# Kernel tuning notes

Hardware: AMD Instinct MI355X
Metric: run time of the kernel (lower is better)

## Reference

```python
import jax, jax.numpy as jnp
import numpy as np

C, T, V, H, DQ = 64, 128, 25, 3, 32  # channels, frames, joints, heads, qkv_dim
EPS = 1e-5
LRELU_SLOPE = 0.1


def pos_embed(channels, num_frames, num_joints):
    # DSTA-Net style sinusoidal Pos_Embed: position index is the joint id, tiled over frames
    pos = np.tile(np.arange(num_joints, dtype=np.float32), num_frames)[:, None]  # (T*V, 1)
    div = np.exp(np.arange(0, channels, 2, dtype=np.float32) * -(np.log(10000.0) / channels))
    pe = np.zeros((num_frames * num_joints, channels), dtype=np.float32)
    pe[:, 0::2] = np.sin(pos * div)
    pe[:, 1::2] = np.cos(pos * div)
    pe = pe.reshape(num_frames, num_joints, channels).transpose(2, 0, 1)[None]  # (1, C, T, V)
    return jnp.asarray(pe)


def batchnorm2d(x, gamma, beta):
    # training-mode BN over (N, T, V) per channel, biased variance (torch default)
    m = x.mean(axis=(0, 2, 3), keepdims=True)
    v = x.var(axis=(0, 2, 3), keepdims=True)
    return (x - m) * jax.lax.rsqrt(v + EPS) * gamma[None, :, None, None] + beta[None, :, None, None]


def setup_inputs() -> dict:
    key = jax.random.key(0)
    ks = jax.random.split(key, 4)
    N = 64
    return {
        "x": jax.random.normal(ks[0], (N, C, T, V), jnp.float32),
        "Wqkv": jax.random.normal(ks[1], (2 * H * DQ, C), jnp.float32) * 0.05,   # 1x1 conv weight
        "bqkv": jnp.zeros((2 * H * DQ,), jnp.float32),
        "alphas": jnp.ones((1, H, 1, 1), jnp.float32),
        "att0s": jax.random.uniform(ks[2], (1, H, V, V), jnp.float32) / V,
        "Wout": jax.random.normal(ks[3], (C, H * C, 1, 5), jnp.float32) * 0.02,  # (1,5) temporal conv
        "bout": jnp.zeros((C,), jnp.float32),
        "gamma": jnp.ones((C,), jnp.float32),
        "beta": jnp.zeros((C,), jnp.float32),
    }


def reference(x, Wqkv, bqkv, alphas, att0s, Wout, bout, gamma, beta):
    N = x.shape[0]
    xs = x + pos_embed(C, T, V)                                   # pes(x) + x
    qk = jnp.einsum('nctv,oc->notv', xs, Wqkv) + bqkv[None, :, None, None]
    qk = qk.reshape(N, 2 * H, DQ, T, V)
    q, k = qk[:, :H], qk[:, H:]
    # tanh-gated joint-attention, no softmax
    att = jnp.tanh(jnp.einsum('nhctu,nhctv->nhuv', q, k) / (DQ * T)) * alphas + att0s
    y = jnp.einsum('nctu,nhuv->nhctv', x, att).reshape(N, H * C, T, V)
    y = jax.lax.conv_general_dilated(
        y, Wout, window_strides=(1, 1), padding=((0, 0), (2, 2)),
        dimension_numbers=('NCHW', 'OIHW', 'NCHW')) + bout[None, :, None, None]
    y = batchnorm2d(y, gamma, beta)
    return jax.nn.leaky_relu(y + x, LRELU_SLOPE)                  # ress is identity (in==out)
```

## Files before the change

### kernel.cpp

```cpp
#include <hip/hip_runtime.h>
#include <hip/hip_bf16.h>


#define WS_ATT    0
#define WS_STATS  120000
#define WS_WBF    120128
#define WS_WP     150848
#define WS_BP     156992
#define WS_PE     157184
#define WS_SPART  158784
#define WS_ATTBF  166976

typedef __attribute__((ext_vector_type(8))) short short8;
typedef __attribute__((ext_vector_type(4))) float floatx4;

__device__ __forceinline__ float us2f(unsigned short u) {
    union { unsigned int i; float f; } w; w.i = ((unsigned int)u) << 16; return w.f;
}
__device__ __forceinline__ unsigned short f2us(float f) {
    __hip_bfloat16_raw r = __float2bfloat16(f); return r.x;
}

__device__ __forceinline__ int swz(int col, int byteoff) {
    return col * 128 + ((((byteoff >> 4) ^ (col & 7)) << 4) | (byteoff & 15));
}

__device__ __forceinline__ void bar_lgkm() {
    asm volatile("s_waitcnt lgkmcnt(0)" ::: "memory");
    __builtin_amdgcn_s_barrier();
}

__global__ void k_wprep(const float* __restrict__ Wout, const float* __restrict__ Wqkv,
                        const float* __restrict__ bqkv, unsigned short* __restrict__ Abf,
                        unsigned short* __restrict__ Wp, float* __restrict__ bp,
                        float* __restrict__ pe)
{
    int i = blockIdx.x * 256 + threadIdx.x;
    if (i < 61440) {
        int tap = i / 12288, rem = i % 12288;
        int o = rem / 192, hc = rem % 192;
        Abf[i] = f2us(Wout[o * 960 + hc * 5 + tap]);
    } else if (i < 73728) {
        int j = i - 61440;
        int np = j >> 6, c = j & 63;
        int h = np >> 6, qk = (np >> 5) & 1, cp = np & 31;
        Wp[j] = f2us(Wqkv[(qk * 96 + h * 32 + cp) * 64 + c]);
    } else if (i < 73920) {
        int np = i - 73728;
        int h = np >> 6, qk = (np >> 5) & 1, cp = np & 31;
        bp[np] = bqkv[qk * 96 + h * 32 + cp];
    } else if (i < 75520) {
        int e = i - 73920;
        int c = e / 25, v = e % 25;
        int ii = c >> 1;
        float d = expf(-(float)(2 * ii) * (9.210340371976184f / 64.0f));
        float a = (float)v * d;
        pe[e] = (c & 1) ? cosf(a) : sinf(a);
    }
}

#define CPAD 112

__global__ __launch_bounds__(256, 2) void k_att(
    const float* __restrict__ x, const unsigned short* __restrict__ Wp,
    const float* __restrict__ bp, const float* __restrict__ peg,
    float* __restrict__ att_raw)
{
    __shared__ unsigned short xs_s[2][CPAD * 64];
    __shared__ unsigned short qk_s[3 * CPAD * 64];
    __shared__ float pe_s[1600];

    const int tid  = threadIdx.x;
    const int lane = tid & 63, wv = tid >> 6;
    const int l16  = lane & 15, quad = lane >> 4;
    const int n    = blockIdx.y;
    const int tb0  = blockIdx.x * 16;

    const int col_a = lane;
    const int col_b = 64 + lane;
    const int va = (col_a < 25) ? col_a : (col_a < 50 ? col_a - 25 : col_a - 50);
    const int vb = (col_b < 75) ? col_b - 50 : col_b - 75;
    char* qkb = (char*)qk_s;

    float ra0[8], ra1[8], rb0[8], rb1[8];

#define LOADCH(CH) do {                                                         \
    const int g0_ = (tb0 + (CH) * 4) * 25;                                      \
    _Pragma("unroll")                                                           \
    for (int cp8 = 0; cp8 < 8; ++cp8) {                                         \
        const float* xp0_ = x + (size_t)(n * 64 + (wv * 8 + cp8) * 2) * 3200 + g0_; \
        const float* xp1_ = xp0_ + 3200;                                        \
        ra0[cp8] = xp0_[col_a]; ra1[cp8] = xp1_[col_a];                         \
        if (lane < 36) { rb0[cp8] = xp0_[col_b]; rb1[cp8] = xp1_[col_b]; }      \
    } } while (0)

    LOADCH(0);

    for (int e = tid; e < 1600; e += 256) pe_s[e] = peg[e];

    short8 afrag[3][2];
    float  biasr[3][4];
    #pragma unroll
    for (int mt = 0; mt < 3; ++mt) {
        int row = (3 * wv + mt) * 16 + l16;
        #pragma unroll
        for (int kk = 0; kk < 2; ++kk)
            afrag[mt][kk] = *(const short8*)(Wp + row * 64 + kk * 32 + quad * 8);
        #pragma unroll
        for (int reg = 0; reg < 4; ++reg)
            biasr[mt][reg] = bp[(3 * wv + mt) * 16 + quad * 4 + reg];
    }

    floatx4 qacc[3][2][2];
    #pragma unroll
    for (int h = 0; h < 3; ++h)
        #pragma unroll
        for (int a = 0; a < 2; ++a)
            #pragma unroll
            for (int b = 0; b < 2; ++b)
                qacc[h][a][b] = (floatx4){0.0f, 0.0f, 0.0f, 0.0f};

    bar_lgkm();

    #pragma unroll
    for (int ch = 0; ch < 4; ++ch) {
        char* xsb = (char*)xs_s[ch & 1];

        #pragma unroll
        for (int cp8 = 0; cp8 < 8; ++cp8) {
            const int cpair = wv * 8 + cp8, c0 = cpair * 2;
            unsigned int pk =
                (unsigned int)f2us(ra0[cp8] + pe_s[c0 * 25 + va]) |
                ((unsigned int)f2us(ra1[cp8] + pe_s[c0 * 25 + 25 + va]) << 16);
            *(unsigned int*)(xsb + swz(col_a, cpair * 4)) = pk;
            if (lane < 36) {
                pk = (unsigned int)f2us(rb0[cp8] + pe_s[c0 * 25 + vb]) |
                     ((unsigned int)f2us(rb1[cp8] + pe_s[c0 * 25 + 25 + vb]) << 16);
                *(unsigned int*)(xsb + swz(col_b, cpair * 4)) = pk;
            }
        }
        if (ch < 3) LOADCH(ch + 1);
        bar_lgkm();

        #pragma unroll
        for (int nt = 0; nt < 7; ++nt) {
            const int col = nt * 16 + l16;
            short8 b0 = *(const short8*)(xsb + swz(col, quad * 16));
            short8 b1 = *(const short8*)(xsb + swz(col, 64 + quad * 16));
            #pragma unroll
            for (int mt = 0; mt < 3; ++mt) {
                floatx4 acc = (floatx4){0.0f, 0.0f, 0.0f, 0.0f};
                acc = __builtin_amdgcn_mfma_f32_16x16x32_bf16(afrag[mt][0], b0, acc, 0, 0, 0);
                acc = __builtin_amdgcn_mfma_f32_16x16x32_bf16(afrag[mt][1], b1, acc, 0, 0, 0);
                const int np  = (3 * wv + mt) * 16 + quad * 4;
                const int h   = np >> 6;
                const int off = (np & 63) * 2;
                unsigned long long pk =
                      (unsigned long long)f2us(acc[0] + biasr[mt][0])
                    | ((unsigned long long)f2us(acc[1] + biasr[mt][1]) << 16)
                    | ((unsigned long long)f2us(acc[2] + biasr[mt][2]) << 32)
                    | ((unsigned long long)f2us(acc[3] + biasr[mt][3]) << 48);
                *(unsigned long long*)(qkb + h * (CPAD * 128) + swz(col, off)) = pk;
            }
        }
        bar_lgkm();

        const int tcol = wv * 25;
        #pragma unroll
        for (int h = 0; h < 3; ++h) {
            char* qh = qkb + h * (CPAD * 128);
            short8 qa0 = *(const short8*)(qh + swz(tcol + l16,      quad * 16));
            short8 qa1 = *(const short8*)(qh + swz(tcol + 16 + l16, quad * 16));
            short8 kb0 = *(const short8*)(qh + swz(tcol + l16,      64 + quad * 16));
            short8 kb1 = *(const short8*)(qh + swz(tcol + 16 + l16, 64 + quad * 16));
            qacc[h][0][0] = __builtin_amdgcn_mfma_f32_16x16x32_bf16(qa0, kb0, qacc[h][0][0], 0, 0, 0);
            qacc[h][0][1] = __builtin_amdgcn_mfma_f32_16x16x32_bf16(qa0, kb1, qacc[h][0][1], 0, 0, 0);
            qacc[h][1][0] = __builtin_amdgcn_mfma_f32_16x16x32_bf16(qa1, kb0, qacc[h][1][0], 0, 0, 0);
            qacc[h][1][1] = __builtin_amdgcn_mfma_f32_16x16x32_bf16(qa1, kb1, qacc[h][1][1], 0, 0, 0);
        }
    }

    __syncthreads();
    float* att_s = (float*)qk_s;
    for (int e = tid; e < 1875; e += 256) att_s[e] = 0.0f;
    __syncthreads();
    #pragma unroll
    for (int h = 0; h < 3; ++h) {
        #pragma unroll
        for (int ut = 0; ut < 2; ++ut) {
            #pragma unroll
            for (int vt = 0; vt < 2; ++vt) {
                const int v = vt * 16 + l16;
                if (v < 25) {
                    const int ub = ut * 16 + quad * 4;
                    #pragma unroll
                    for (int reg = 0; reg < 4; ++reg) {
                        const int u = ub + reg;
                        if (u < 25)
                            atomicAdd(&att_s[h * 625 + u * 25 + v], qacc[h][ut][vt][reg]);
                    }
                }
            }
        }
    }
    __syncthreads();
    for (int e = tid; e < 1875; e += 256)
        atomicAdd(&att_raw[(size_t)n * 1875 + e], att_s[e]);
}

__global__ void k_attfin(const float* __restrict__ att_raw,
                         unsigned short* __restrict__ attbf,
                         const float* __restrict__ alphas,
                         const float* __restrict__ att0s)
{
    int idx = blockIdx.x * 256 + threadIdx.x;
    if (idx >= 64 * 3 * 25 * 40) return;
    int u = idx % 40;
    int r = idx / 40;
    int v = r % 25;
    int nh = r / 25;
    int h = nh % 3;
    unsigned short val = 0;
    if (u < 25) {
        float a = att_raw[nh * 625 + u * 25 + v];
        val = f2us(tanhf(a * (1.0f / 4096.0f)) * alphas[h] + att0s[h * 625 + u * 25 + v]);
    }
    attbf[idx] = val;
}

__global__ __launch_bounds__(256, 3) void k_conv(
    const float* __restrict__ x, const unsigned short* __restrict__ Abf,
    const float* __restrict__ bout, const unsigned short* __restrict__ attbf,
    float* __restrict__ out, float* __restrict__ spart)
{
    __shared__ unsigned short yT[11136];
    __shared__ unsigned short x_sb[4096];
    __shared__ unsigned short attT[3000];
    __shared__ float stats_s[128];

    const int tid = threadIdx.x;
    const int n = blockIdx.y;
    const int t0 = blockIdx.x * 2;
    char* xsb = (char*)x_sb;

    if (tid < 128) stats_s[tid] = 0.0f;

    for (int e = tid; e < 896; e += 256) {
        int c = e / 14, r = e % 14;
        int t = r / 7, u = 25 + r % 7;
        *(unsigned short*)(xsb + swz(c, (t * 32 + u) * 2)) = 0;
    }
    for (int e = tid; e < 1600; e += 256) {
        int c = e / 25, j = e % 25;
        const float2 xv = *(const float2*)(x + (size_t)(n * 64 + c) * 3200 + t0 * 25 + 2 * j);
        int i0 = 2 * j, i1 = i0 + 1;
        int p0 = (i0 / 25) * 32 + (i0 % 25);
        int p1 = (i1 / 25) * 32 + (i1 % 25);
        *(unsigned short*)(xsb + swz(c, p0 * 2)) = f2us(xv.x);
        *(unsigned short*)(xsb + swz(c, p1 * 2)) = f2us(xv.y);
    }
    {
        const uint4* src = (const uint4*)(attbf + (size_t)n * 3000);
        uint4* dst = (uint4*)attT;
        for (int e = tid; e < 375; e += 256) dst[e] = src[e];
    }
    for (int e = tid; e < 1536; e += 256) {
        int t = e / 768, r = e % 768;
        int vi = r / 192, hc = r % 192;
        int vv = (vi < 2) ? vi : (25 + vi);
        int phys = (t * 29 + vv) * 192 + (((hc >> 3) ^ (vv & 7)) << 3) + (hc & 7);
        yT[phys] = 0;
    }
    __syncthreads();

    const int lane = tid & 63, wv = tid >> 6;
    const int quad = lane >> 4, l16 = lane & 15;

    {
        const int c0 = wv * 16;
        const int crow = c0 + l16;
        short8 af[2];
        #pragma unroll
        for (int t = 0; t < 2; ++t)
            af[t] = *(const short8*)(xsb + swz(crow, (t * 32 + quad * 8) * 2));
        short8 bfr[3][2];
        #pragma unroll
        for (int h = 0; h < 3; ++h)
            #pragma unroll
            for (int nt = 0; nt < 2; ++nt) {
                int v = nt * 16 + l16; if (v > 24) v = 24;
                bfr[h][nt] = *(const short8*)&attT[(h * 25 + v) * 40 + quad * 8];
            }
        #pragma unroll
        for (int t = 0; t < 2; ++t)
            #pragma unroll
            for (int h = 0; h < 3; ++h)
                #pragma unroll
                for (int nt = 0; nt < 2; ++nt) {
                    floatx4 d = (floatx4){0.0f, 0.0f, 0.0f, 0.0f};
                    d = __builtin_amdgcn_mfma_f32_16x16x32_bf16(af[t], bfr[h][nt], d, 0, 0, 0);
                    const int v = nt * 16 + l16;
                    if (v < 25) {
                        const int vv = v + 2;
                        const int hc = h * 64 + c0 + quad * 4;
                        const int phys = (t * 29 + vv) * 192 + (((hc >> 3) ^ (vv & 7)) << 3) + (hc & 7);
                        unsigned long long pk =
                              (unsigned long long)f2us(d[0])
                            | ((unsigned long long)f2us(d[1]) << 16)
                            | ((unsigned long long)f2us(d[2]) << 32)
                            | ((unsigned long long)f2us(d[3]) << 48);
                        *(unsigned long long*)&yT[phys] = pk;
                    }
                }
    }

    const int o0 = wv * 16;
    short8 areg[5][6];
    const unsigned short* apb = Abf + (o0 + l16) * 192 + quad * 8;
    #pragma unroll
    for (int tap = 0; tap < 5; ++tap)
        #pragma unroll
        for (int kk = 0; kk < 6; ++kk)
            areg[tap][kk] = *(const short8*)(apb + tap * 12288 + kk * 32);
    float bo[4];
    #pragma unroll
    for (int reg = 0; reg < 4; ++reg) bo[reg] = bout[o0 + quad * 4 + reg];

    bar_lgkm();

    float s1[4] = {0, 0, 0, 0}, s2[4] = {0, 0, 0, 0};
    #pragma unroll
    for (int nt = 0; nt < 4; ++nt) {
        int col = nt * 16 + l16;
        const bool ok = col < 50;
        if (col > 49) col = 49;
        const int tc = col / 25, vc = col % 25;
        floatx4 acc = (floatx4){0.0f, 0.0f, 0.0f, 0.0f};
        #pragma unroll
        for (int tap = 0; tap < 5; ++tap) {
            const int vv = vc + tap;
            const int ro = (tc * 29 + vv) * 192, vx = vv & 7;
            #pragma unroll
            for (int kk = 0; kk < 6; ++kk) {
                short8 b = *(const short8*)&yT[ro + (((kk * 4 + quad) ^ vx) << 3)];
                acc = __builtin_amdgcn_mfma_f32_16x16x32_bf16(areg[tap][kk], b, acc, 0, 0, 0);
            }
        }
        float vr[4];
        #pragma unroll
        for (int reg = 0; reg < 4; ++reg)
            vr[reg] = ok ? acc[reg] + bo[reg] : 0.0f;
        if (ok) {
            float* op = out + (size_t)(n * 64 + o0 + quad * 4) * 3200 + (t0 + tc) * 25 + vc;
            #pragma unroll
            for (int reg = 0; reg < 4; ++reg)
                op[(size_t)reg * 3200] = vr[reg];
        }
        #pragma unroll
        for (int reg = 0; reg < 4; ++reg) {
            s1[reg] += vr[reg];
            s2[reg] = fmaf(vr[reg], vr[reg], s2[reg]);
        }
    }

    #pragma unroll
    for (int reg = 0; reg < 4; ++reg) {
        float a = s1[reg], b = s2[reg];
        #pragma unroll
        for (int m = 1; m < 16; m <<= 1) {
            a += __shfl_xor(a, m);
            b += __shfl_xor(b, m);
        }
        if (l16 == 0) {
            atomicAdd(&stats_s[o0 + quad * 4 + reg], a);
            atomicAdd(&stats_s[64 + o0 + quad * 4 + reg], b);
        }
    }
    __syncthreads();
    if (tid < 128)
        atomicAdd(&spart[(size_t)blockIdx.x * 128 + tid], stats_s[tid]);
}

__global__ void k_statsred(const float* __restrict__ spart, float* __restrict__ stats)
{
    int o = threadIdx.x;
    float s = 0.0f;
    #pragma unroll 8
    for (int t = 0; t < 64; ++t) s += spart[t * 128 + o];
    stats[o] = s;
}

__global__ void k_final(const float* __restrict__ stats, const float4* __restrict__ x4,
                        const float* __restrict__ gamma, const float* __restrict__ beta,
                        float4* __restrict__ out4)
{
    int idx = blockIdx.x * 256 + threadIdx.x;
    if (idx >= 3276800) return;
    int o = (idx / 800) & 63;
    const float inv = 1.0f / 204800.0f;
    float m   = stats[o] * inv;
    float ex2 = stats[64 + o] * inv;
    float var = ex2 - m * m;
    float r = rsqrtf(var + 1e-5f);
    float g = gamma[o], bb = beta[o];
    float4 v = out4[idx];
    float4 xx = x4[idx];
    float4 res;
    float t;
    t = (v.x - m) * r * g + bb + xx.x; res.x = fmaxf(t, 0.1f * t);
    t = (v.y - m) * r * g + bb + xx.y; res.y = fmaxf(t, 0.1f * t);
    t = (v.z - m) * r * g + bb + xx.z; res.z = fmaxf(t, 0.1f * t);
    t = (v.w - m) * r * g + bb + xx.w; res.w = fmaxf(t, 0.1f * t);
    out4[idx] = res;
}

extern "C" void kernel_launch(void* const* d_in, const int* in_sizes, int n_in,
                              void* d_out, int out_size, void* d_ws, size_t ws_size,
                              hipStream_t stream)
{
    const float* x      = (const float*)d_in[0];
    const float* Wqkv   = (const float*)d_in[1];
    const float* bqkv   = (const float*)d_in[2];
    const float* alphas = (const float*)d_in[3];
    const float* att0s  = (const float*)d_in[4];
    const float* Wout   = (const float*)d_in[5];
    const float* bout   = (const float*)d_in[6];
    const float* gamma  = (const float*)d_in[7];
    const float* beta   = (const float*)d_in[8];
    float* ws  = (float*)d_ws;
    float* out = (float*)d_out;
    unsigned short* Abf   = (unsigned short*)(ws + WS_WBF);
    unsigned short* Wp    = (unsigned short*)(ws + WS_WP);
    float*          bp    = ws + WS_BP;
    float*          pe    = ws + WS_PE;
    float*          spart = ws + WS_SPART;
    unsigned short* attbf = (unsigned short*)(ws + WS_ATTBF);

    hipMemsetAsync(d_ws, 0, (size_t)120000 * sizeof(float), stream);
    hipMemsetAsync(spart, 0, (size_t)8192 * sizeof(float), stream);

    k_wprep   <<<296, 256, 0, stream>>>(Wout, Wqkv, bqkv, Abf, Wp, bp, pe);
    k_att     <<<dim3(8, 64),  256, 0, stream>>>(x, Wp, bp, pe, ws + WS_ATT);
    k_attfin  <<<750, 256, 0, stream>>>(ws + WS_ATT, attbf, alphas, att0s);
    k_conv    <<<dim3(64, 64), 256, 0, stream>>>(x, Abf, bout, attbf, out, spart);
    k_statsred<<<1, 128, 0, stream>>>(spart, ws + WS_STATS);
    k_final   <<<12800, 256, 0, stream>>>(ws + WS_STATS, (const float4*)x,
                                          gamma, beta, (float4*)out);
}
```

Before: 268.5 us.

## Drop register prefetch and double buffer in k_att, compute pos-embed in-kernel

The attention-score kernel no longer prefetches the next chunk of x into registers or double-buffers the x tile in shared memory. It now loads each chunk directly and uses full __syncthreads barriers instead of the custom lgkm barrier. The sinusoidal position embedding is computed per block with expf/sinf/cosf rather than read from the workspace, and att_s gets its own shared buffer. This lowers register and LDS pressure, which may help occupancy, but it gives up global-load/compute overlap and adds transcendental math to every block.

```diff
diff --git a/kernel.cpp b/kernel.cpp
--- a/kernel.cpp
+++ b/kernel.cpp
@@ -63,12 +63,12 @@
 
 __global__ __launch_bounds__(256, 2) void k_att(
     const float* __restrict__ x, const unsigned short* __restrict__ Wp,
-    const float* __restrict__ bp, const float* __restrict__ peg,
-    float* __restrict__ att_raw)
-{
-    __shared__ unsigned short xs_s[2][CPAD * 64];
+    const float* __restrict__ bp, float* __restrict__ att_raw)
+{
+    __shared__ unsigned short xs_s[CPAD * 64];
     __shared__ unsigned short qk_s[3 * CPAD * 64];
     __shared__ float pe_s[1600];
+    __shared__ float att_s[1875];
 
     const int tid  = threadIdx.x;
     const int lane = tid & 63, wv = tid >> 6;
@@ -76,71 +76,69 @@
     const int n    = blockIdx.y;
     const int tb0  = blockIdx.x * 16;
 
+    for (int e = tid; e < 1600; e += 256) {
+        int c = e / 25, v = e % 25;
+        int i = c >> 1;
+        float d = expf(-(float)(2 * i) * (9.210340371976184f / 64.0f));
+        float a = (float)v * d;
+        pe_s[e] = (c & 1) ? cosf(a) : sinf(a);
+    }
+    for (int e = tid; e < 1875; e += 256) att_s[e] = 0.0f;
+
+    short8 afrag[3][2];
+    float  biasr[3][4];
+    #pragma unroll
+    for (int mt = 0; mt < 3; ++mt) {
+        int row = (3 * wv + mt) * 16 + l16;
+        #pragma unroll
+        for (int kk = 0; kk < 2; ++kk)
+            afrag[mt][kk] = *(const short8*)(Wp + row * 64 + kk * 32 + quad * 8);
+        #pragma unroll
+        for (int reg = 0; reg < 4; ++reg)
+            biasr[mt][reg] = bp[(3 * wv + mt) * 16 + quad * 4 + reg];
+    }
+
+    floatx4 qacc[3][2][2];
+    #pragma unroll
+    for (int h = 0; h < 3; ++h)
+        #pragma unroll
+        for (int a = 0; a < 2; ++a)
+            #pragma unroll
+            for (int b = 0; b < 2; ++b)
+                qacc[h][a][b] = (floatx4){0.0f, 0.0f, 0.0f, 0.0f};
+
     const int col_a = lane;
     const int col_b = 64 + lane;
     const int va = (col_a < 25) ? col_a : (col_a < 50 ? col_a - 25 : col_a - 50);
     const int vb = (col_b < 75) ? col_b - 50 : col_b - 75;
+    char* xsb = (char*)xs_s;
     char* qkb = (char*)qk_s;
 
-    float ra0[8], ra1[8], rb0[8], rb1[8];
-
-#define LOADCH(CH) do {                                                         \
-    const int g0_ = (tb0 + (CH) * 4) * 25;                                      \
-    _Pragma("unroll")                                                           \
-    for (int cp8 = 0; cp8 < 8; ++cp8) {                                         \
-        const float* xp0_ = x + (size_t)(n * 64 + (wv * 8 + cp8) * 2) * 3200 + g0_; \
-        const float* xp1_ = xp0_ + 3200;                                        \
-        ra0[cp8] = xp0_[col_a]; ra1[cp8] = xp1_[col_a];                         \
-        if (lane < 36) { rb0[cp8] = xp0_[col_b]; rb1[cp8] = xp1_[col_b]; }      \
-    } } while (0)
-
-    LOADCH(0);
-
-    for (int e = tid; e < 1600; e += 256) pe_s[e] = peg[e];
-
-    short8 afrag[3][2];
-    float  biasr[3][4];
-    #pragma unroll
-    for (int mt = 0; mt < 3; ++mt) {
-        int row = (3 * wv + mt) * 16 + l16;
-        #pragma unroll
-        for (int kk = 0; kk < 2; ++kk)
-            afrag[mt][kk] = *(const short8*)(Wp + row * 64 + kk * 32 + quad * 8);
-        #pragma unroll
-        for (int reg = 0; reg < 4; ++reg)
-            biasr[mt][reg] = bp[(3 * wv + mt) * 16 + quad * 4 + reg];
-    }
-
-    floatx4 qacc[3][2][2];
-    #pragma unroll
-    for (int h = 0; h < 3; ++h)
-        #pragma unroll
-        for (int a = 0; a < 2; ++a)
-            #pragma unroll
-            for (int b = 0; b < 2; ++b)
-                qacc[h][a][b] = (floatx4){0.0f, 0.0f, 0.0f, 0.0f};
-
-    bar_lgkm();
-
-    #pragma unroll
+    __syncthreads();
+
     for (int ch = 0; ch < 4; ++ch) {
-        char* xsb = (char*)xs_s[ch & 1];
+        const int g0 = (tb0 + ch * 4) * 25;
 
         #pragma unroll
         for (int cp8 = 0; cp8 < 8; ++cp8) {
-            const int cpair = wv * 8 + cp8, c0 = cpair * 2;
-            unsigned int pk =
-                (unsigned int)f2us(ra0[cp8] + pe_s[c0 * 25 + va]) |
-                ((unsigned int)f2us(ra1[cp8] + pe_s[c0 * 25 + 25 + va]) << 16);
-            *(unsigned int*)(xsb + swz(col_a, cpair * 4)) = pk;
+            const int cpair = wv * 8 + cp8;
+            const int c0 = cpair * 2;
+            const float* xp0 = x + (size_t)(n * 64 + c0) * 3200 + g0;
+            const float* xp1 = xp0 + 3200;
+            {
+                unsigned int pk =
+                    (unsigned int)f2us(xp0[col_a] + pe_s[c0 * 25 + va]) |
+                    ((unsigned int)f2us(xp1[col_a] + pe_s[c0 * 25 + 25 + va]) << 16);
+                *(unsigned int*)(xsb + swz(col_a, cpair * 4)) = pk;
+            }
             if (lane < 36) {
-                pk = (unsigned int)f2us(rb0[cp8] + pe_s[c0 * 25 + vb]) |
-                     ((unsigned int)f2us(rb1[cp8] + pe_s[c0 * 25 + 25 + vb]) << 16);
+                unsigned int pk =
+                    (unsigned int)f2us(xp0[col_b] + pe_s[c0 * 25 + vb]) |
+                    ((unsigned int)f2us(xp1[col_b] + pe_s[c0 * 25 + 25 + vb]) << 16);
                 *(unsigned int*)(xsb + swz(col_b, cpair * 4)) = pk;
             }
         }
-        if (ch < 3) LOADCH(ch + 1);
-        bar_lgkm();
+        __syncthreads();
 
         #pragma unroll
         for (int nt = 0; nt < 7; ++nt) {
@@ -163,7 +161,7 @@
                 *(unsigned long long*)(qkb + h * (CPAD * 128) + swz(col, off)) = pk;
             }
         }
-        bar_lgkm();
+        __syncthreads();
 
         const int tcol = wv * 25;
         #pragma unroll
@@ -180,10 +178,6 @@
         }
     }
 
-    __syncthreads();
-    float* att_s = (float*)qk_s;
-    for (int e = tid; e < 1875; e += 256) att_s[e] = 0.0f;
-    __syncthreads();
     #pragma unroll
     for (int h = 0; h < 3; ++h) {
         #pragma unroll
@@ -440,7 +434,7 @@
     hipMemsetAsync(spart, 0, (size_t)8192 * sizeof(float), stream);
 
     k_wprep   <<<296, 256, 0, stream>>>(Wout, Wqkv, bqkv, Abf, Wp, bp, pe);
-    k_att     <<<dim3(8, 64),  256, 0, stream>>>(x, Wp, bp, pe, ws + WS_ATT);
+    k_att     <<<dim3(8, 64),  256, 0, stream>>>(x, Wp, bp, ws + WS_ATT);
     k_attfin  <<<750, 256, 0, stream>>>(ws + WS_ATT, attbf, alphas, att0s);
     k_conv    <<<dim3(64, 64), 256, 0, stream>>>(x, Abf, bout, attbf, out, spart);
     k_statsred<<<1, 128, 0, stream>>>(spart, ws + WS_STATS);
```

Result: slower. 294.5 us (+9.7%).
